# Kernel optimization log

Hardware: AMD Instinct MI355X
Metric: run time of the kernel (lower is better)

## Reference

```python
import jax, jax.numpy as jnp
import numpy as np

IGNORE = -100000.0

def setup_inputs() -> dict:
    key = jax.random.key(0)
    ks = jax.random.split(key, 5)
    B, S, E, H, D = 4, 2048, 1024, 16, 64
    return {
        "x": jax.random.normal(ks[0], (B, S, E), dtype=jnp.float32),
        "W_Q": jax.random.normal(ks[1], (H, E, D), dtype=jnp.float32) * (E ** -0.5),
        "W_K": jax.random.normal(ks[2], (H, E, D), dtype=jnp.float32) * (E ** -0.5),
        "W_V": jax.random.normal(ks[3], (H, E, D), dtype=jnp.float32) * (E ** -0.5),
        "W_O": jax.random.normal(ks[4], (H, D, E), dtype=jnp.float32) * (D ** -0.5),
        "is_causal": 1,
    }

def reference(x, W_Q, W_K, W_V, W_O, is_causal):
    d_head = W_Q.shape[-1]
    # projections: [b, p, n_heads, d_head]
    q = jnp.einsum('nmd,bpm->bpnd', W_Q, x)
    k = jnp.einsum('nmd,bpm->bpnd', W_K, x)
    v = jnp.einsum('nmd,bpm->bpnd', W_V, x)
    # scores: [b, n_heads, q_pos, k_pos]
    scores = jnp.einsum('bqnd,bknd->bnqk', q, k) / np.sqrt(d_head).astype(jnp.float32)
    if is_causal:
        S = scores.shape[-1]
        mask = jnp.triu(jnp.ones((S, S), dtype=bool), k=1)  # True above diagonal
        scores = jnp.where(mask, jnp.float32(IGNORE), scores)
    attn = jax.nn.softmax(scores, axis=-1)
    # weighted values: [b, q_pos, n_heads, d_head]
    z = jnp.einsum('bknd,bnqk->bqnd', v, attn)
    # output projection: [b, q_pos, embed_dim]
    o = jnp.einsum('ndm,bqnd->bqm', W_O, z)
    # average_attn_weights=True -> mean over heads
    return o, attn.mean(axis=1)
```

## Files before the change

### kernel.cpp

```cpp
#include <hip/hip_runtime.h>
#include <stdint.h>


#define BB 4
#define SS 2048
#define EE 1024
#define HH 16
#define DD 64
#define MTOT (BB*SS)
#define HD (HH*DD)
#define QKV_ELEMS ((size_t)MTOT*HD)

typedef float f32x4 __attribute__((ext_vector_type(4)));
typedef short bf16x8 __attribute__((ext_vector_type(8)));

#define GLL(g, l) __builtin_amdgcn_global_load_lds( \
    (const __attribute__((address_space(1))) void*)(g), \
    (__attribute__((address_space(3))) void*)(l), 16, 0, 0)

__device__ __forceinline__ short f2bf(float f) {
    unsigned u = __builtin_bit_cast(unsigned, f);
    u += 0x7FFFu + ((u >> 16) & 1u);
    return (short)(u >> 16);
}

__global__ __launch_bounds__(256) void k_xcast(const float* __restrict__ x,
                                               short* __restrict__ xbf) {
    int i = blockIdx.x*256 + threadIdx.x;
    float4 f = ((const float4*)x)[i];
    short4 s; s.x=f2bf(f.x); s.y=f2bf(f.y); s.z=f2bf(f.z); s.w=f2bf(f.w);
    ((short4*)xbf)[i] = s;
}

__global__ __launch_bounds__(256) void k_wprep(const float* __restrict__ wq,
        const float* __restrict__ wk, const float* __restrict__ wv,
        const float* __restrict__ wo, short* __restrict__ wtq,
        short* __restrict__ wto) {
    __shared__ short Tl[64][72];
    int t = threadIdx.x, x = blockIdx.x, y = blockIdx.y;
    int r4 = t >> 2, c4 = (t & 3) << 4;
    if (y < 48) {
        int which = y >> 4, h = y & 15, e0 = x*64;
        const float* src = (which==0?wq:which==1?wk:wv) + (size_t)h*EE*DD;
        const float* p = src + (size_t)(e0 + r4)*DD + c4;
        #pragma unroll
        for (int j = 0; j < 4; ++j) {
            float4 f = ((const float4*)p)[j];
            Tl[r4][c4+j*4+0]=f2bf(f.x); Tl[r4][c4+j*4+1]=f2bf(f.y);
            Tl[r4][c4+j*4+2]=f2bf(f.z); Tl[r4][c4+j*4+3]=f2bf(f.w);
        }
        __syncthreads();
        size_t nrow = ((size_t)(which*16 + h))*64 + r4;
        #pragma unroll
        for (int i = 0; i < 16; ++i)
            wtq[nrow*1024 + e0 + c4 + i] = Tl[c4+i][r4];
    } else {
        int h = y - 48, e0 = x*64;
        const float* src = wo + (size_t)h*DD*EE;
        const float* p = src + (size_t)r4*EE + e0 + c4;
        #pragma unroll
        for (int j = 0; j < 4; ++j) {
            float4 f = ((const float4*)p)[j];
            Tl[r4][c4+j*4+0]=f2bf(f.x); Tl[r4][c4+j*4+1]=f2bf(f.y);
            Tl[r4][c4+j*4+2]=f2bf(f.z); Tl[r4][c4+j*4+3]=f2bf(f.w);
        }
        __syncthreads();
        #pragma unroll
        for (int i = 0; i < 16; ++i)
            wto[(size_t)(e0 + r4)*1024 + h*64 + c4 + i] = Tl[c4+i][r4];
    }
}

__global__ __launch_bounds__(256) void k_proj(const short* __restrict__ xbf,
        const short* __restrict__ wtq, short* __restrict__ qkv) {
    __shared__ short As[128*64];
    __shared__ short Bs[128*64];
    int t = threadIdx.x;
    int m0 = blockIdx.x*128, n0 = blockIdx.y*128;
    int lane = t & 63, l15 = lane & 15, quad = lane >> 4;
    int wm = (t>>6) >> 1, wn = (t>>6) & 1;
    f32x4 acc[4][4];
    #pragma unroll
    for (int i=0;i<4;++i)
        #pragma unroll
        for (int c=0;c<4;++c) acc[i][c] = (f32x4){0,0,0,0};

    for (int k0 = 0; k0 < EE; k0 += 64) {
        __syncthreads();
        #pragma unroll
        for (int j = 0; j < 4; ++j) {
            int c = j*256 + t;
            int row = c >> 3, cg = c & 7;
            GLL(xbf + (size_t)(m0+row)*EE + k0 + cg*8, &As[(j*256 + (t & 192))*8]);
            GLL(wtq + (size_t)(n0+row)*EE + k0 + cg*8, &Bs[(j*256 + (t & 192))*8]);
        }
        __syncthreads();
        #pragma unroll
        for (int kp = 0; kp < 64; kp += 32)
            #pragma unroll
            for (int i = 0; i < 4; ++i) {
                bf16x8 a = *(const bf16x8*)&As[(wm*64 + i*16 + l15)*64 + kp + quad*8];
                #pragma unroll
                for (int c = 0; c < 4; ++c) {
                    bf16x8 b = *(const bf16x8*)&Bs[(wn*64 + c*16 + l15)*64 + kp + quad*8];
                    acc[i][c] = __builtin_amdgcn_mfma_f32_16x16x32_bf16(a, b, acc[i][c], 0, 0, 0);
                }
            }
    }
    short* vt = qkv + 2*QKV_ELEMS;
    #pragma unroll
    for (int i = 0; i < 4; ++i)
        #pragma unroll
        for (int c = 0; c < 4; ++c) {
            int n = n0 + wn*64 + c*16 + l15;
            int row = m0 + wm*64 + i*16 + quad*4;
            if (n < 2048) {
                #pragma unroll
                for (int r = 0; r < 4; ++r)
                    qkv[(size_t)(n>>10)*QKV_ELEMS + (size_t)(row+r)*HD + (n & 1023)] =
                        f2bf(acc[i][c][r]);
            } else {
                short4 s4;
                s4.x = f2bf(acc[i][c][0]); s4.y = f2bf(acc[i][c][1]);
                s4.z = f2bf(acc[i][c][2]); s4.w = f2bf(acc[i][c][3]);
                int bb_ = row >> 11, pos = row & 2047;
                *(short4*)&vt[((size_t)bb_*HD + (n - 2048))*SS + pos] = s4;
            }
        }
}

__global__ __launch_bounds__(256) void k_attnz(const short* __restrict__ qws,
        const short* __restrict__ kws, const short* __restrict__ vtg,
        short* __restrict__ zws, float* __restrict__ c2ws) {
    __shared__ short Ks[64][72];
    __shared__ short Vt[64][72];
    __shared__ short Ps[4][32][72];
    int t = threadIdx.x;
    int h = blockIdx.y, b = blockIdx.z;
    int w = t>>6, lane = t&63, l15 = lane&15, quad = lane>>4;
    int sr = t>>2, sc = (t&3)<<4;

    const short* ksrc = kws + (size_t)(b*SS + sr)*HD + h*DD + sc;
    const short* vsrc = vtg + ((size_t)b*HD + h*DD + sr)*SS + sc;

    bf16x8 ones;
    #pragma unroll
    for (int i=0;i<8;++i) ones[i] = (short)0x3F80;
    const float SC = 0.125f * 1.4426950408889634f;

    for (int half = 0; half < 2; ++half) {
        int qx = half ? (15 - (int)blockIdx.x) : (int)blockIdx.x;
        int q0 = qx*128;

        bf16x8 qr[2][2];
        #pragma unroll
        for (int mf=0; mf<2; ++mf)
            #pragma unroll
            for (int kp=0; kp<2; ++kp)
                qr[mf][kp] = *(const bf16x8*)(qws +
                    (size_t)(b*SS + q0 + w*32 + mf*16 + l15)*HD + h*DD + kp*32 + quad*8);

        f32x4 accz[2][4];
        f32x4 accl[2];
        #pragma unroll
        for (int mf=0;mf<2;++mf) {
            accl[mf] = (f32x4){0,0,0,0};
            #pragma unroll
            for (int c=0;c<4;++c) accz[mf][c] = (f32x4){0,0,0,0};
        }
        int nk = q0/64 + 2;
        int qmax = q0 + w*32 + 31;

        uint4 pk0 = ((const uint4*)ksrc)[0], pk1 = ((const uint4*)ksrc)[1];
        uint4 pv0 = ((const uint4*)vsrc)[0], pv1 = ((const uint4*)vsrc)[1];

        for (int kt = 0; kt < nk; ++kt) {
            int k0 = kt*64;
            __syncthreads();
            *(uint4*)&Ks[sr][sc]   = pk0;  *(uint4*)&Ks[sr][sc+8] = pk1;
            *(uint4*)&Vt[sr][sc]   = pv0;  *(uint4*)&Vt[sr][sc+8] = pv1;
            __syncthreads();
            if (kt+1 < nk) {
                const uint4* kn = (const uint4*)(ksrc + (size_t)(k0+64)*HD);
                const uint4* vn = (const uint4*)(vsrc + (k0+64));
                pk0=kn[0]; pk1=kn[1]; pv0=vn[0]; pv1=vn[1];
            }
            if (k0 > qmax) continue;

            f32x4 s[2][4];
            #pragma unroll
            for (int mf=0;mf<2;++mf)
                #pragma unroll
                for (int c=0;c<4;++c) s[mf][c] = (f32x4){0,0,0,0};
            __builtin_amdgcn_s_setprio(1);
            #pragma unroll
            for (int c=0;c<4;++c)
                #pragma unroll
                for (int kp=0;kp<2;++kp) {
                    bf16x8 aK = *(const bf16x8*)&Ks[c*16+l15][kp*32+quad*8];
                    s[0][c] = __builtin_amdgcn_mfma_f32_16x16x32_bf16(aK, qr[0][kp], s[0][c], 0, 0, 0);
                    s[1][c] = __builtin_amdgcn_mfma_f32_16x16x32_bf16(aK, qr[1][kp], s[1][c], 0, 0, 0);
                }
            __builtin_amdgcn_s_setprio(0);
            #pragma unroll
            for (int mf=0;mf<2;++mf) {
                int qg = q0 + w*32 + mf*16 + l15;
                #pragma unroll
                for (int c=0;c<4;++c) {
                    int kb = k0 + c*16 + quad*4;
                    short4 s4;
                    #pragma unroll
                    for (int r=0;r<4;++r) {
                        float p_ = (kb + r <= qg) ? __builtin_amdgcn_exp2f(s[mf][c][r]*SC) : 0.0f;
                        ((short*)&s4)[r] = f2bf(p_);
                    }
                    *(short4*)&Ps[w][mf*16 + l15][c*16 + quad*4] = s4;
                }
            }
            __builtin_amdgcn_s_setprio(1);
            #pragma unroll
            for (int kp=0;kp<2;++kp) {
                bf16x8 pa0 = *(const bf16x8*)&Ps[w][l15][kp*32+quad*8];
                bf16x8 pa1 = *(const bf16x8*)&Ps[w][16+l15][kp*32+quad*8];
                #pragma unroll
                for (int cc=0;cc<4;++cc) {
                    bf16x8 vb = *(const bf16x8*)&Vt[cc*16+l15][kp*32+quad*8];
                    accz[0][cc] = __builtin_amdgcn_mfma_f32_16x16x32_bf16(pa0, vb, accz[0][cc], 0, 0, 0);
                    accz[1][cc] = __builtin_amdgcn_mfma_f32_16x16x32_bf16(pa1, vb, accz[1][cc], 0, 0, 0);
                }
                accl[0] = __builtin_amdgcn_mfma_f32_16x16x32_bf16(pa0, ones, accl[0], 0, 0, 0);
                accl[1] = __builtin_amdgcn_mfma_f32_16x16x32_bf16(pa1, ones, accl[1], 0, 0, 0);
            }
            __builtin_amdgcn_s_setprio(0);
        }
        #pragma unroll
        for (int mf=0;mf<2;++mf) {
            float il[4];
            #pragma unroll
            for (int r=0;r<4;++r) il[r] = 1.0f / accl[mf][r];
            #pragma unroll
            for (int cc=0;cc<4;++cc)
                #pragma unroll
                for (int r=0;r<4;++r) {
                    int row = q0 + w*32 + mf*16 + quad*4 + r;
                    zws[(size_t)(b*SS+row)*HD + h*DD + cc*16 + l15] = f2bf(accz[mf][cc][r]*il[r]);
                }
            if (l15 == 0) {
                size_t base = ((size_t)(b*HH+h))*SS + q0 + w*32 + mf*16 + quad*4;
                #pragma unroll
                for (int r=0;r<4;++r)
                    c2ws[base+r] = __log2f(accl[mf][r]);
            }
        }
    }
}

__global__ __launch_bounds__(256) void k_mean(const short* __restrict__ qws,
        const short* __restrict__ kws, const float* __restrict__ c2ws,
        float* __restrict__ attn_out) {
    int b = blockIdx.z;
    int qx = (b & 1) ? (31 - (int)blockIdx.x) : (int)blockIdx.x;
    int q0 = qx*64, k0 = blockIdx.y*64;
    int t = threadIdx.x;
    if (k0 > q0) {
        int r = t >> 2, cq = (t & 3) << 4;
        float4 z4 = {0.f,0.f,0.f,0.f};
        float* dst = attn_out + ((size_t)(b*SS + q0 + r))*SS + k0 + cq;
        #pragma unroll
        for (int j = 0; j < 4; ++j) ((float4*)dst)[j] = z4;
        return;
    }
    __shared__ short Ksm[2][64][72];
    __shared__ float c2s[16][64];
    int w = t>>6, lane = t&63, l15 = lane&15, quad = lane>>4;
    int sr = t>>2, sc = (t&3)<<4;
    #pragma unroll
    for (int i = 0; i < 4; ++i) {
        int idx = t + i*256;
        int hh = idx >> 6, r = idx & 63;
        c2s[hh][r] = c2ws[((size_t)(b*HH+hh))*SS + q0 + r];
    }
    const short* ksrc = kws + (size_t)(b*SS + k0 + sr)*HD + sc;
    const short* qsrc = qws + (size_t)(b*SS + q0 + w*16 + l15)*HD + quad*8;

    {
        const uint4* kp = (const uint4*)ksrc;
        uint4 c = kp[0], d = kp[1];
        *(uint4*)&Ksm[0][sr][sc] = c;  *(uint4*)&Ksm[0][sr][sc+8] = d;
    }
    bf16x8 qc0 = *(const bf16x8*)(qsrc);
    bf16x8 qc1 = *(const bf16x8*)(qsrc + 32);

    const float SC = 0.125f * 1.4426950408889634f;
    int rowg0 = q0 + w*16 + quad*4;
    f32x4 acc[4] = { {0,0,0,0},{0,0,0,0},{0,0,0,0},{0,0,0,0} };

    for (int h = 0; h < HH; ++h) {
        int cur = h & 1;
        __syncthreads();
        uint4 nka, nkb; bf16x8 nq0, nq1;
        if (h < HH-1) {
            const uint4* kn = (const uint4*)(ksrc + (h+1)*64);
            nka = kn[0]; nkb = kn[1];
            nq0 = *(const bf16x8*)(qsrc + (h+1)*64);
            nq1 = *(const bf16x8*)(qsrc + (h+1)*64 + 32);
        }

        f32x4 c2 = *(const f32x4*)&c2s[h][w*16 + quad*4];
        #pragma unroll
        for (int ns = 0; ns < 4; ++ns) {
            bf16x8 b0 = *(const bf16x8*)&Ksm[cur][ns*16+l15][quad*8];
            bf16x8 b1 = *(const bf16x8*)&Ksm[cur][ns*16+l15][quad*8+32];
            f32x4 s = {0,0,0,0};
            s = __builtin_amdgcn_mfma_f32_16x16x32_bf16(qc0, b0, s, 0, 0, 0);
            s = __builtin_amdgcn_mfma_f32_16x16x32_bf16(qc1, b1, s, 0, 0, 0);
            int col = k0 + ns*16 + l15;
            #pragma unroll
            for (int r = 0; r < 4; ++r) {
                float ex = __builtin_amdgcn_exp2f(s[r]*SC - c2[r]);
                acc[ns][r] += (col <= rowg0 + r) ? ex : 0.0f;
            }
        }

        if (h < HH-1) {
            int nxt = cur ^ 1;
            *(uint4*)&Ksm[nxt][sr][sc]   = nka;  *(uint4*)&Ksm[nxt][sr][sc+8] = nkb;
            qc0 = nq0; qc1 = nq1;
        }
    }
    #pragma unroll
    for (int ns = 0; ns < 4; ++ns)
        #pragma unroll
        for (int r = 0; r < 4; ++r)
            attn_out[((size_t)(b*SS + rowg0 + r))*SS + k0 + ns*16 + l15] =
                acc[ns][r] * 0.0625f;
}

__global__ __launch_bounds__(256) void k_oproj(const short* __restrict__ zws,
        const short* __restrict__ wto, float* __restrict__ outp) {
    __shared__ short As[128*64];
    __shared__ short Bs[128*64];
    int t = threadIdx.x;
    int m0 = blockIdx.x*128, n0 = blockIdx.y*128;
    int lane = t & 63, l15 = lane & 15, quad = lane >> 4;
    int wm = (t>>6) >> 1, wn = (t>>6) & 1;
    f32x4 acc[4][4];
    #pragma unroll
    for (int i=0;i<4;++i)
        #pragma unroll
        for (int c=0;c<4;++c) acc[i][c] = (f32x4){0,0,0,0};

    for (int k0 = 0; k0 < HD; k0 += 64) {
        __syncthreads();
        #pragma unroll
        for (int j = 0; j < 4; ++j) {
            int c = j*256 + t;
            int row = c >> 3, cg = c & 7;
            GLL(zws + (size_t)(m0+row)*HD + k0 + cg*8, &As[(j*256 + (t & 192))*8]);
            GLL(wto + (size_t)(n0+row)*HD + k0 + cg*8, &Bs[(j*256 + (t & 192))*8]);
        }
        __syncthreads();
        #pragma unroll
        for (int kp = 0; kp < 64; kp += 32)
            #pragma unroll
            for (int i = 0; i < 4; ++i) {
                bf16x8 a = *(const bf16x8*)&As[(wm*64 + i*16 + l15)*64 + kp + quad*8];
                #pragma unroll
                for (int c = 0; c < 4; ++c) {
                    bf16x8 b = *(const bf16x8*)&Bs[(wn*64 + c*16 + l15)*64 + kp + quad*8];
                    acc[i][c] = __builtin_amdgcn_mfma_f32_16x16x32_bf16(a, b, acc[i][c], 0, 0, 0);
                }
            }
    }
    #pragma unroll
    for (int i = 0; i < 4; ++i)
        #pragma unroll
        for (int c = 0; c < 4; ++c)
            #pragma unroll
            for (int r = 0; r < 4; ++r) {
                int row = m0 + wm*64 + i*16 + quad*4 + r;
                int n = n0 + wn*64 + c*16 + l15;
                outp[(size_t)row*EE + n] = acc[i][c][r];
            }
}

extern "C" void kernel_launch(void* const* d_in, const int* in_sizes, int n_in,
                              void* d_out, int out_size, void* d_ws, size_t ws_size,
                              hipStream_t stream) {
    const float* x  = (const float*)d_in[0];
    const float* wq = (const float*)d_in[1];
    const float* wk = (const float*)d_in[2];
    const float* wv = (const float*)d_in[3];
    const float* wo = (const float*)d_in[4];

    short* xbf = (short*)d_ws;
    short* qb  = xbf + QKV_ELEMS;
    short* kb  = qb + QKV_ELEMS;
    short* vtb = kb + QKV_ELEMS;
    short* wtq = vtb + QKV_ELEMS;
    short* wto = wtq + (size_t)3*1024*1024;
    float* c2w = (float*)(wto + (size_t)1024*1024);
    short* zb  = xbf;

    float* o = (float*)d_out;
    float* attn_out = o + (size_t)MTOT*EE;

    k_xcast<<<dim3(8192),     256, 0, stream>>>(x, xbf);
    k_wprep<<<dim3(16,64),    256, 0, stream>>>(wq, wk, wv, wo, wtq, wto);
    k_proj <<<dim3(64,24),    256, 0, stream>>>(xbf, wtq, qb);
    k_attnz<<<dim3(8,16,4),   256, 0, stream>>>(qb, kb, vtb, zb, c2w);
    k_mean <<<dim3(32,32,4),  256, 0, stream>>>(qb, kb, c2w, attn_out);
    k_oproj<<<dim3(64,8),     256, 0, stream>>>(zb, wto, o);
}
```

Baseline: 371.5 us.

## Double-buffer shared-memory tiles in projection, attention and output GEMM kernels

Adds a second LDS buffer to the QKV projection, attention and output projection kernels. The global-to-LDS load for the next k-tile is issued before the MFMA work on the current tile, and one __syncthreads per iteration is dropped. The aim is to hide global memory latency behind matrix math and cut barrier stalls. In exchange, LDS use per block doubles (64 KB in the GEMMs), which may lower occupancy.

```diff
diff --git a/kernel.cpp b/kernel.cpp
--- a/kernel.cpp
+++ b/kernel.cpp
@@ -73,8 +73,8 @@
 
 __global__ __launch_bounds__(256) void k_proj(const short* __restrict__ xbf,
         const short* __restrict__ wtq, short* __restrict__ qkv) {
-    __shared__ short As[128*64];
-    __shared__ short Bs[128*64];
+    __shared__ short As[2][128*64];
+    __shared__ short Bs[2][128*64];
     int t = threadIdx.x;
     int m0 = blockIdx.x*128, n0 = blockIdx.y*128;
     int lane = t & 63, l15 = lane & 15, quad = lane >> 4;
@@ -85,24 +85,34 @@
         #pragma unroll
         for (int c=0;c<4;++c) acc[i][c] = (f32x4){0,0,0,0};
 
-    for (int k0 = 0; k0 < EE; k0 += 64) {
+    #pragma unroll
+    for (int j = 0; j < 4; ++j) {
+        int c = j*256 + t;
+        int row = c >> 3, cg = c & 7;
+        GLL(xbf + (size_t)(m0+row)*EE + cg*8, &As[0][(j*256 + (t & 192))*8]);
+        GLL(wtq + (size_t)(n0+row)*EE + cg*8, &Bs[0][(j*256 + (t & 192))*8]);
+    }
+    for (int kt = 0; kt < 16; ++kt) {
+        int cur = kt & 1;
         __syncthreads();
-        #pragma unroll
-        for (int j = 0; j < 4; ++j) {
-            int c = j*256 + t;
-            int row = c >> 3, cg = c & 7;
-            GLL(xbf + (size_t)(m0+row)*EE + k0 + cg*8, &As[(j*256 + (t & 192))*8]);
-            GLL(wtq + (size_t)(n0+row)*EE + k0 + cg*8, &Bs[(j*256 + (t & 192))*8]);
-        }
-        __syncthreads();
+        if (kt < 15) {
+            int k0n = (kt+1)*64;
+            #pragma unroll
+            for (int j = 0; j < 4; ++j) {
+                int c = j*256 + t;
+                int row = c >> 3, cg = c & 7;
+                GLL(xbf + (size_t)(m0+row)*EE + k0n + cg*8, &As[cur^1][(j*256 + (t & 192))*8]);
+                GLL(wtq + (size_t)(n0+row)*EE + k0n + cg*8, &Bs[cur^1][(j*256 + (t & 192))*8]);
+            }
+        }
         #pragma unroll
         for (int kp = 0; kp < 64; kp += 32)
             #pragma unroll
             for (int i = 0; i < 4; ++i) {
-                bf16x8 a = *(const bf16x8*)&As[(wm*64 + i*16 + l15)*64 + kp + quad*8];
+                bf16x8 a = *(const bf16x8*)&As[cur][(wm*64 + i*16 + l15)*64 + kp + quad*8];
                 #pragma unroll
                 for (int c = 0; c < 4; ++c) {
-                    bf16x8 b = *(const bf16x8*)&Bs[(wn*64 + c*16 + l15)*64 + kp + quad*8];
+                    bf16x8 b = *(const bf16x8*)&Bs[cur][(wn*64 + c*16 + l15)*64 + kp + quad*8];
                     acc[i][c] = __builtin_amdgcn_mfma_f32_16x16x32_bf16(a, b, acc[i][c], 0, 0, 0);
                 }
             }
@@ -132,8 +142,8 @@
 __global__ __launch_bounds__(256) void k_attnz(const short* __restrict__ qws,
         const short* __restrict__ kws, const short* __restrict__ vtg,
         short* __restrict__ zws, float* __restrict__ c2ws) {
-    __shared__ short Ks[64][72];
-    __shared__ short Vt[64][72];
+    __shared__ short Ks[2][64][72];
+    __shared__ short Vt[2][64][72];
     __shared__ short Ps[4][32][72];
     int t = threadIdx.x;
     int h = blockIdx.y, b = blockIdx.z;
@@ -173,65 +183,70 @@
 
         uint4 pk0 = ((const uint4*)ksrc)[0], pk1 = ((const uint4*)ksrc)[1];
         uint4 pv0 = ((const uint4*)vsrc)[0], pv1 = ((const uint4*)vsrc)[1];
+        if (half) __syncthreads();
+        *(uint4*)&Ks[0][sr][sc] = pk0;  *(uint4*)&Ks[0][sr][sc+8] = pk1;
+        *(uint4*)&Vt[0][sr][sc] = pv0;  *(uint4*)&Vt[0][sr][sc+8] = pv1;
 
         for (int kt = 0; kt < nk; ++kt) {
+            int cur = kt & 1;
             int k0 = kt*64;
-            __syncthreads();
-            *(uint4*)&Ks[sr][sc]   = pk0;  *(uint4*)&Ks[sr][sc+8] = pk1;
-            *(uint4*)&Vt[sr][sc]   = pv0;  *(uint4*)&Vt[sr][sc+8] = pv1;
             __syncthreads();
             if (kt+1 < nk) {
                 const uint4* kn = (const uint4*)(ksrc + (size_t)(k0+64)*HD);
                 const uint4* vn = (const uint4*)(vsrc + (k0+64));
                 pk0=kn[0]; pk1=kn[1]; pv0=vn[0]; pv1=vn[1];
             }
-            if (k0 > qmax) continue;
-
-            f32x4 s[2][4];
-            #pragma unroll
-            for (int mf=0;mf<2;++mf)
-                #pragma unroll
-                for (int c=0;c<4;++c) s[mf][c] = (f32x4){0,0,0,0};
-            __builtin_amdgcn_s_setprio(1);
-            #pragma unroll
-            for (int c=0;c<4;++c)
+            if (k0 <= qmax) {
+                f32x4 s[2][4];
+                #pragma unroll
+                for (int mf=0;mf<2;++mf)
+                    #pragma unroll
+                    for (int c=0;c<4;++c) s[mf][c] = (f32x4){0,0,0,0};
+                __builtin_amdgcn_s_setprio(1);
+                #pragma unroll
+                for (int c=0;c<4;++c)
+                    #pragma unroll
+                    for (int kp=0;kp<2;++kp) {
+                        bf16x8 aK = *(const bf16x8*)&Ks[cur][c*16+l15][kp*32+quad*8];
+                        s[0][c] = __builtin_amdgcn_mfma_f32_16x16x32_bf16(aK, qr[0][kp], s[0][c], 0, 0, 0);
+                        s[1][c] = __builtin_amdgcn_mfma_f32_16x16x32_bf16(aK, qr[1][kp], s[1][c], 0, 0, 0);
+                    }
+                __builtin_amdgcn_s_setprio(0);
+                #pragma unroll
+                for (int mf=0;mf<2;++mf) {
+                    int qg = q0 + w*32 + mf*16 + l15;
+                    #pragma unroll
+                    for (int c=0;c<4;++c) {
+                        int kb = k0 + c*16 + quad*4;
+                        short4 s4;
+                        #pragma unroll
+                        for (int r=0;r<4;++r) {
+                            float p_ = (kb + r <= qg) ? __builtin_amdgcn_exp2f(s[mf][c][r]*SC) : 0.0f;
+                            ((short*)&s4)[r] = f2bf(p_);
+                        }
+                        *(short4*)&Ps[w][mf*16 + l15][c*16 + quad*4] = s4;
+                    }
+                }
+                __builtin_amdgcn_s_setprio(1);
                 #pragma unroll
                 for (int kp=0;kp<2;++kp) {
-                    bf16x8 aK = *(const bf16x8*)&Ks[c*16+l15][kp*32+quad*8];
-                    s[0][c] = __builtin_amdgcn_mfma_f32_16x16x32_bf16(aK, qr[0][kp], s[0][c], 0, 0, 0);
-                    s[1][c] = __builtin_amdgcn_mfma_f32_16x16x32_bf16(aK, qr[1][kp], s[1][c], 0, 0, 0);
+                    bf16x8 pa0 = *(const bf16x8*)&Ps[w][l15][kp*32+quad*8];
+                    bf16x8 pa1 = *(const bf16x8*)&Ps[w][16+l15][kp*32+quad*8];
+                    #pragma unroll
+                    for (int cc=0;cc<4;++cc) {
+                        bf16x8 vb = *(const bf16x8*)&Vt[cur][cc*16+l15][kp*32+quad*8];
+                        accz[0][cc] = __builtin_amdgcn_mfma_f32_16x16x32_bf16(pa0, vb, accz[0][cc], 0, 0, 0);
+                        accz[1][cc] = __builtin_amdgcn_mfma_f32_16x16x32_bf16(pa1, vb, accz[1][cc], 0, 0, 0);
+                    }
+                    accl[0] = __builtin_amdgcn_mfma_f32_16x16x32_bf16(pa0, ones, accl[0], 0, 0, 0);
+                    accl[1] = __builtin_amdgcn_mfma_f32_16x16x32_bf16(pa1, ones, accl[1], 0, 0, 0);
                 }
-            __builtin_amdgcn_s_setprio(0);
-            #pragma unroll
-            for (int mf=0;mf<2;++mf) {
-                int qg = q0 + w*32 + mf*16 + l15;
-                #pragma unroll
-                for (int c=0;c<4;++c) {
-                    int kb = k0 + c*16 + quad*4;
-                    short4 s4;
-                    #pragma unroll
-                    for (int r=0;r<4;++r) {
-                        float p_ = (kb + r <= qg) ? __builtin_amdgcn_exp2f(s[mf][c][r]*SC) : 0.0f;
-                        ((short*)&s4)[r] = f2bf(p_);
-                    }
-                    *(short4*)&Ps[w][mf*16 + l15][c*16 + quad*4] = s4;
-                }
-            }
-            __builtin_amdgcn_s_setprio(1);
-            #pragma unroll
-            for (int kp=0;kp<2;++kp) {
-                bf16x8 pa0 = *(const bf16x8*)&Ps[w][l15][kp*32+quad*8];
-                bf16x8 pa1 = *(const bf16x8*)&Ps[w][16+l15][kp*32+quad*8];
-                #pragma unroll
-                for (int cc=0;cc<4;++cc) {
-                    bf16x8 vb = *(const bf16x8*)&Vt[cc*16+l15][kp*32+quad*8];
-                    accz[0][cc] = __builtin_amdgcn_mfma_f32_16x16x32_bf16(pa0, vb, accz[0][cc], 0, 0, 0);
-                    accz[1][cc] = __builtin_amdgcn_mfma_f32_16x16x32_bf16(pa1, vb, accz[1][cc], 0, 0, 0);
-                }
-                accl[0] = __builtin_amdgcn_mfma_f32_16x16x32_bf16(pa0, ones, accl[0], 0, 0, 0);
-                accl[1] = __builtin_amdgcn_mfma_f32_16x16x32_bf16(pa1, ones, accl[1], 0, 0, 0);
-            }
-            __builtin_amdgcn_s_setprio(0);
+                __builtin_amdgcn_s_setprio(0);
+            }
+            if (kt+1 < nk) {
+                *(uint4*)&Ks[cur^1][sr][sc] = pk0;  *(uint4*)&Ks[cur^1][sr][sc+8] = pk1;
+                *(uint4*)&Vt[cur^1][sr][sc] = pv0;  *(uint4*)&Vt[cur^1][sr][sc+8] = pv1;
+            }
         }
         #pragma unroll
         for (int mf=0;mf<2;++mf) {
@@ -338,8 +353,8 @@
 
 __global__ __launch_bounds__(256) void k_oproj(const short* __restrict__ zws,
         const short* __restrict__ wto, float* __restrict__ outp) {
-    __shared__ short As[128*64];
-    __shared__ short Bs[128*64];
+    __shared__ short As[2][128*64];
+    __shared__ short Bs[2][128*64];
     int t = threadIdx.x;
     int m0 = blockIdx.x*128, n0 = blockIdx.y*128;
     int lane = t & 63, l15 = lane & 15, quad = lane >> 4;
@@ -350,24 +365,34 @@
         #pragma unroll
         for (int c=0;c<4;++c) acc[i][c] = (f32x4){0,0,0,0};
 
-    for (int k0 = 0; k0 < HD; k0 += 64) {
+    #pragma unroll
+    for (int j = 0; j < 4; ++j) {
+        int c = j*256 + t;
+        int row = c >> 3, cg = c & 7;
+        GLL(zws + (size_t)(m0+row)*HD + cg*8, &As[0][(j*256 + (t & 192))*8]);
+        GLL(wto + (size_t)(n0+row)*HD + cg*8, &Bs[0][(j*256 + (t & 192))*8]);
+    }
+    for (int kt = 0; kt < 16; ++kt) {
+        int cur = kt & 1;
         __syncthreads();
-        #pragma unroll
-        for (int j = 0; j < 4; ++j) {
-            int c = j*256 + t;
-            int row = c >> 3, cg = c & 7;
-            GLL(zws + (size_t)(m0+row)*HD + k0 + cg*8, &As[(j*256 + (t & 192))*8]);
-            GLL(wto + (size_t)(n0+row)*HD + k0 + cg*8, &Bs[(j*256 + (t & 192))*8]);
-        }
-        __syncthreads();
+        if (kt < 15) {
+            int k0n = (kt+1)*64;
+            #pragma unroll
+            for (int j = 0; j < 4; ++j) {
+                int c = j*256 + t;
+                int row = c >> 3, cg = c & 7;
+                GLL(zws + (size_t)(m0+row)*HD + k0n + cg*8, &As[cur^1][(j*256 + (t & 192))*8]);
+                GLL(wto + (size_t)(n0+row)*HD + k0n + cg*8, &Bs[cur^1][(j*256 + (t & 192))*8]);
+            }
+        }
         #pragma unroll
         for (int kp = 0; kp < 64; kp += 32)
             #pragma unroll
             for (int i = 0; i < 4; ++i) {
-                bf16x8 a = *(const bf16x8*)&As[(wm*64 + i*16 + l15)*64 + kp + quad*8];
+                bf16x8 a = *(const bf16x8*)&As[cur][(wm*64 + i*16 + l15)*64 + kp + quad*8];
                 #pragma unroll
                 for (int c = 0; c < 4; ++c) {
-                    bf16x8 b = *(const bf16x8*)&Bs[(wn*64 + c*16 + l15)*64 + kp + quad*8];
+                    bf16x8 b = *(const bf16x8*)&Bs[cur][(wn*64 + c*16 + l15)*64 + kp + quad*8];
                     acc[i][c] = __builtin_amdgcn_mfma_f32_16x16x32_bf16(a, b, acc[i][c], 0, 0, 0);
                 }
             }
```

Measured after the change: 388.8 us. +4.6%, slower.
